# Performance work log

Measured on AMD Instinct MI355X. Metric: run time of the kernel, lower is better.

Reference implementation:

```python
import jax, jax.numpy as jnp
import numpy as np

IN, ENC, H = 60, 32, 64  # input feat, encoder out, LSTM hidden per direction


def _lstm_scan(x_tbf, W_ih, W_hh, b):
    """x_tbf: [T,B,ENC]. Returns final (h, c), each [B,H]. PyTorch gate order i,f,g,o."""
    B = x_tbf.shape[1]
    h0 = jnp.zeros((B, H), x_tbf.dtype)
    c0 = jnp.zeros((B, H), x_tbf.dtype)

    def step(carry, x_t):
        h, c = carry
        gates = x_t @ W_ih.T + h @ W_hh.T + b  # [B, 4H]
        i, f, g, o = jnp.split(gates, 4, axis=-1)
        c = jax.nn.sigmoid(f) * c + jax.nn.sigmoid(i) * jnp.tanh(g)
        h = jax.nn.sigmoid(o) * jnp.tanh(c)
        return (h, c), None

    (h_fin, c_fin), _ = jax.lax.scan(step, (h0, c0), x_tbf)
    return h_fin, c_fin


def setup_inputs() -> dict:
    key = jax.random.key(0)
    ks = jax.random.split(key, 10)
    B, T = 256, 4096
    s_enc = 1.0 / np.sqrt(IN)
    s_lstm = 1.0 / np.sqrt(H)
    s_fin = 1.0 / np.sqrt(2 * H)
    return {
        "c": jax.random.normal(ks[0], (B, T, IN), jnp.float32),
        "W_enc": jax.random.uniform(ks[1], (ENC, IN), jnp.float32, -s_enc, s_enc),
        "b_enc": jax.random.uniform(ks[2], (ENC,), jnp.float32, -s_enc, s_enc),
        "W_ih_f": jax.random.uniform(ks[3], (4 * H, ENC), jnp.float32, -s_lstm, s_lstm),
        "W_hh_f": jax.random.uniform(ks[4], (4 * H, H), jnp.float32, -s_lstm, s_lstm),
        "b_f": jax.random.uniform(ks[5], (4 * H,), jnp.float32, -s_lstm, s_lstm),
        "W_ih_b": jax.random.uniform(ks[6], (4 * H, ENC), jnp.float32, -s_lstm, s_lstm),
        "W_hh_b": jax.random.uniform(ks[7], (4 * H, H), jnp.float32, -s_lstm, s_lstm),
        "b_b": jax.random.uniform(ks[8], (4 * H,), jnp.float32, -s_lstm, s_lstm),
        "W_fin": jax.random.uniform(ks[9], (3, 2 * H), jnp.float32, -s_fin, s_fin),
        "b_fin": jnp.zeros((3,), jnp.float32),
    }


def reference(c, W_enc, b_enc, W_ih_f, W_hh_f, b_f, W_ih_b, W_hh_b, b_b, W_fin, b_fin):
    # SequenceWise linear encoder: [B,T,60] -> [B,T,32]
    x = c @ W_enc.T + b_enc
    x_tbf = jnp.transpose(x, (1, 0, 2))  # [T,B,ENC]
    # Bidirectional LSTM; original code unpacks (h_n, c_n) as (c, h),
    # so it feeds the final CELL states into final_fc — reproduce that.
    _, c_fwd = _lstm_scan(x_tbf, W_ih_f, W_hh_f, b_f)
    _, c_bwd = _lstm_scan(x_tbf[::-1], W_ih_b, W_hh_b, b_b)
    hidden = jnp.concatenate([c_fwd, c_bwd], axis=1)  # [B, 2H]
    return hidden @ W_fin.T + b_fin  # [B, 3]
```

## Files before the change

kernel.cpp:

```cpp
#include <hip/hip_runtime.h>
#include <hip/hip_bf16.h>

#define T_LEN 4096

typedef __attribute__((ext_vector_type(8))) short bfrag8;
typedef __attribute__((ext_vector_type(4))) float f32x4;

__device__ __forceinline__ void wg_barrier() {
  asm volatile("s_waitcnt lgkmcnt(0)\ns_barrier" ::: "memory");
}

__device__ __forceinline__ float fact(float x, float S, float A, float B) {
  float e = __builtin_amdgcn_exp2f(S * x);
  return A + B * __builtin_amdgcn_rcpf(1.0f + e);
}
__device__ __forceinline__ float ftanh(float x) {
  float e = __builtin_amdgcn_exp2f(2.8853900817779268f * x);
  return 1.0f - 2.0f * __builtin_amdgcn_rcpf(1.0f + e);
}
template <int SEL>
__device__ __forceinline__ float qb(float v) {
  union { float f; int i; } u;
  u.f = v;
  u.i = __builtin_amdgcn_mov_dpp(u.i, SEL * 0x55, 0xF, 0xF, true);
  return u.f;
}

__global__ void prep_enc(const float* __restrict__ W_enc,
                         __hip_bfloat16* __restrict__ Wencb) {
  int u = threadIdx.x;
  if (u < 32) {
    for (int k = 0; k < 64; ++k)
      Wencb[u * 64 + k] = __float2bfloat16(k < 60 ? W_enc[u * 60 + k] : 0.0f);
  }
}

__global__ __launch_bounds__(256) void encoder(const float* __restrict__ c,
                                               const __hip_bfloat16* __restrict__ Wencb,
                                               __hip_bfloat16* __restrict__ x) {
  const int lane = threadIdx.x & 63, wave = threadIdx.x >> 6;
  const int q = lane >> 4, l15 = lane & 15;
  const size_t r0 = ((size_t)blockIdx.x * 4 + wave) * 16;

  bfrag8 bf00 = *(const bfrag8*)(Wencb + (0 * 16 + l15) * 64 + 0 * 32 + q * 8);
  bfrag8 bf01 = *(const bfrag8*)(Wencb + (0 * 16 + l15) * 64 + 1 * 32 + q * 8);
  bfrag8 bf10 = *(const bfrag8*)(Wencb + (1 * 16 + l15) * 64 + 0 * 32 + q * 8);
  bfrag8 bf11 = *(const bfrag8*)(Wencb + (1 * 16 + l15) * 64 + 1 * 32 + q * 8);

  const float* cr = c + (r0 + l15) * 60;
  float4 a0 = *(const float4*)(cr + q * 8);
  float4 a1 = *(const float4*)(cr + q * 8 + 4);
  float4 a2 = *(const float4*)(cr + 32 + q * 8);
  float4 a3 = (q == 3) ? float4{0.f, 0.f, 0.f, 0.f}
                       : *(const float4*)(cr + 36 + q * 8);
  union { bfrag8 v; __hip_bfloat16 h[8]; } A0, A1;
  A0.h[0] = __float2bfloat16(a0.x); A0.h[1] = __float2bfloat16(a0.y);
  A0.h[2] = __float2bfloat16(a0.z); A0.h[3] = __float2bfloat16(a0.w);
  A0.h[4] = __float2bfloat16(a1.x); A0.h[5] = __float2bfloat16(a1.y);
  A0.h[6] = __float2bfloat16(a1.z); A0.h[7] = __float2bfloat16(a1.w);
  A1.h[0] = __float2bfloat16(a2.x); A1.h[1] = __float2bfloat16(a2.y);
  A1.h[2] = __float2bfloat16(a2.z); A1.h[3] = __float2bfloat16(a2.w);
  A1.h[4] = __float2bfloat16(a3.x); A1.h[5] = __float2bfloat16(a3.y);
  A1.h[6] = __float2bfloat16(a3.z); A1.h[7] = __float2bfloat16(a3.w);

  f32x4 acc0 = {0.f, 0.f, 0.f, 0.f}, acc1 = {0.f, 0.f, 0.f, 0.f};
  acc0 = __builtin_amdgcn_mfma_f32_16x16x32_bf16(A0.v, bf00, acc0, 0, 0, 0);
  acc1 = __builtin_amdgcn_mfma_f32_16x16x32_bf16(A0.v, bf10, acc1, 0, 0, 0);
  acc0 = __builtin_amdgcn_mfma_f32_16x16x32_bf16(A1.v, bf01, acc0, 0, 0, 0);
  acc1 = __builtin_amdgcn_mfma_f32_16x16x32_bf16(A1.v, bf11, acc1, 0, 0, 0);

#pragma unroll
  for (int r = 0; r < 4; ++r) {
    size_t row = r0 + q * 4 + r;
    x[row * 32 + l15]      = __float2bfloat16(acc0[r]);
    x[row * 32 + 16 + l15] = __float2bfloat16(acc1[r]);
  }
}

__global__ void prep_weights(const float* __restrict__ b_enc,
                             const float* __restrict__ W_ih_f,
                             const float* __restrict__ W_hh_f,
                             const float* __restrict__ b_f,
                             const float* __restrict__ W_ih_b,
                             const float* __restrict__ W_hh_b,
                             const float* __restrict__ b_b,
                             __hip_bfloat16* __restrict__ Wc,
                             float* __restrict__ biasc) {
  const int dir = blockIdx.x;
  const int np = threadIdx.x;
  const int tile = np >> 4, cc = np & 15;
  const int unit = tile * 4 + (cc >> 2);
  const int gate = cc & 3;
  const int no = gate * 64 + unit;
  const float* W_ih = dir ? W_ih_b : W_ih_f;
  const float* W_hh = dir ? W_hh_b : W_hh_f;
  const float* bv = dir ? b_b : b_f;
  __hip_bfloat16* row = Wc + (size_t)(dir * 256 + np) * 96;
#pragma unroll
  for (int k = 0; k < 32; ++k) row[k] = __float2bfloat16(W_ih[no * 32 + k]);
#pragma unroll
  for (int j = 0; j < 64; ++j) row[32 + j] = __float2bfloat16(W_hh[no * 64 + j]);
  float bb = bv[no];
#pragma unroll
  for (int e = 0; e < 32; ++e) bb += W_ih[no * 32 + e] * b_enc[e];
  biasc[dir * 256 + np] = bb;
}

__global__ __launch_bounds__(512, 2) void lstm_main(
    const __hip_bfloat16* __restrict__ x, const __hip_bfloat16* __restrict__ Wc,
    const float* __restrict__ biasc, float* __restrict__ cfin) {
  __shared__ __align__(16) short Hbuf[2][2][72];

  const int tid = threadIdx.x, lane = tid & 63, wave = tid >> 6;
  const int quad = lane >> 4, l15 = lane & 15;
  const int g = lane & 3;
  const int tsel = quad & 1;
  const int br = quad >> 1;
  const int unit = wave * 8 + tsel * 4 + (l15 >> 2);
  const int dir = (int)blockIdx.x & 1;
  const int pair = (int)blockIdx.x >> 1;
  const int b0 = pair * 2;
  const int bl = b0 + (l15 & 1);

  bfrag8 wf[2][3];
  float bias[2];
#pragma unroll
  for (int tl = 0; tl < 2; ++tl) {
    const int np = wave * 32 + tl * 16 + l15;
    const __hip_bfloat16* wr = Wc + (size_t)(dir * 256 + np) * 96 + quad * 8;
#pragma unroll
    for (int kt = 0; kt < 3; ++kt) wf[tl][kt] = *(const bfrag8*)(wr + kt * 32);
    bias[tl] = biasc[dir * 256 + np];
  }
  const f32x4 bv0 = {bias[0], bias[0], bias[0], bias[0]};
  const f32x4 bv1 = {bias[1], bias[1], bias[1], bias[1]};

  const bool isg = (g == 2);
  const float S = isg ? 2.8853900817779268f : -1.4426950408889634f;
  const float Aa = isg ? 1.0f : 0.0f;
  const float Bb = isg ? -2.0f : 1.0f;

  const __hip_bfloat16* xr = x + (size_t)bl * T_LEN * 32 + quad * 8;

  if (tid < 288) ((short*)Hbuf)[tid] = 0;

  bfrag8 xb[4];
#pragma unroll
  for (int qq = 0; qq < 4; ++qq) {
    int tp = dir ? (T_LEN - 1 - qq) : qq;
    xb[qq] = *(const bfrag8*)(xr + (size_t)tp * 32);
  }

  float cst = 0.f;
  wg_barrier();

#pragma unroll 4
  for (int t = 0; t < T_LEN; ++t) {
    const int cur = t & 1;
    const short* hb = &Hbuf[cur][l15 & 1][0];
    bfrag8 ahA = *(const bfrag8*)(hb + quad * 8);
    bfrag8 ahB = *(const bfrag8*)(hb + 32 + quad * 8);
    f32x4 a0 = __builtin_amdgcn_mfma_f32_16x16x32_bf16(xb[t & 3], wf[0][0], bv0, 0, 0, 0);
    f32x4 a1 = __builtin_amdgcn_mfma_f32_16x16x32_bf16(xb[t & 3], wf[1][0], bv1, 0, 0, 0);
    a0 = __builtin_amdgcn_mfma_f32_16x16x32_bf16(ahA, wf[0][1], a0, 0, 0, 0);
    a1 = __builtin_amdgcn_mfma_f32_16x16x32_bf16(ahA, wf[1][1], a1, 0, 0, 0);
    a0 = __builtin_amdgcn_mfma_f32_16x16x32_bf16(ahB, wf[0][2], a0, 0, 0, 0);
    a1 = __builtin_amdgcn_mfma_f32_16x16x32_bf16(ahB, wf[1][2], a1, 0, 0, 0);
    {
      int tn = t + 4; if (tn > T_LEN - 1) tn = T_LEN - 1;
      int tp = dir ? (T_LEN - 1 - tn) : tn;
      xb[t & 3] = *(const bfrag8*)(xr + (size_t)tp * 32);
    }
    float v0 = tsel ? a1[0] : a0[0];
    float v1 = tsel ? a1[1] : a0[1];
    float v = (quad & 2) ? v1 : v0;
    float act = fact(v, S, Aa, Bb);
    float gi = qb<0>(act), gf = qb<1>(act), gg = qb<2>(act), go = qb<3>(act);
    cst = gf * cst + gi * gg;
    float h = go * ftanh(cst);
    if (g == 0) *(__hip_bfloat16*)&Hbuf[cur ^ 1][br][unit] = __float2bfloat16(h);
    wg_barrier();
  }

  if (g == 0) cfin[(size_t)(dir * 256 + b0 + br) * 64 + unit] = cst;
}

__global__ void final_fc(const float* __restrict__ cfin,
                         const float* __restrict__ W_fin,
                         const float* __restrict__ b_fin,
                         float* __restrict__ out) {
  int b = threadIdx.x;
  const float* cf = cfin + (size_t)b * 64;
  const float* cb = cfin + (size_t)(256 + b) * 64;
  float a0 = b_fin[0], a1 = b_fin[1], a2 = b_fin[2];
  for (int u = 0; u < 64; ++u) {
    float vf = cf[u], vb = cb[u];
    a0 += W_fin[0 * 128 + u] * vf + W_fin[0 * 128 + 64 + u] * vb;
    a1 += W_fin[1 * 128 + u] * vf + W_fin[1 * 128 + 64 + u] * vb;
    a2 += W_fin[2 * 128 + u] * vf + W_fin[2 * 128 + 64 + u] * vb;
  }
  out[b * 3 + 0] = a0;
  out[b * 3 + 1] = a1;
  out[b * 3 + 2] = a2;
}

extern "C" void kernel_launch(void* const* d_in, const int* in_sizes, int n_in,
                              void* d_out, int out_size, void* d_ws, size_t ws_size,
                              hipStream_t stream) {
  (void)in_sizes; (void)n_in; (void)out_size; (void)ws_size;
  const float* c      = (const float*)d_in[0];
  const float* W_enc  = (const float*)d_in[1];
  const float* b_enc  = (const float*)d_in[2];
  const float* W_ih_f = (const float*)d_in[3];
  const float* W_hh_f = (const float*)d_in[4];
  const float* b_f    = (const float*)d_in[5];
  const float* W_ih_b = (const float*)d_in[6];
  const float* W_hh_b = (const float*)d_in[7];
  const float* b_b    = (const float*)d_in[8];
  const float* W_fin  = (const float*)d_in[9];
  const float* b_fin  = (const float*)d_in[10];
  float* out = (float*)d_out;

  char* ws = (char*)d_ws;
  __hip_bfloat16* x     = (__hip_bfloat16*)ws;
  __hip_bfloat16* Wc    = (__hip_bfloat16*)(ws + 67108864);
  float* biasc          = (float*)(ws + 67108864 + 98304);
  __hip_bfloat16* Wencb = (__hip_bfloat16*)(ws + 67108864 + 100352);
  float* cfin           = (float*)(ws + 67108864 + 104448);

  prep_enc<<<1, 32, 0, stream>>>(W_enc, Wencb);
  prep_weights<<<2, 256, 0, stream>>>(b_enc, W_ih_f, W_hh_f, b_f,
                                      W_ih_b, W_hh_b, b_b, Wc, biasc);
  encoder<<<16384, 256, 0, stream>>>(c, Wencb, x);
  lstm_main<<<256, 512, 0, stream>>>(x, Wc, biasc, cfin);
  final_fc<<<1, 256, 0, stream>>>(cfin, W_fin, b_fin, out);
}
```

Before: 1.324 ms.

## Fold encoder linear into LSTM input weights and read raw input directly

Precomputes W_ih·W_enc so the LSTM input projection consumes the raw 60-feature input directly, removing the separate encoder kernel and its intermediate bf16 activation buffer. The recurrent kernel now loads fp32 rows of c, converts them to bf16 in-loop, and does one extra pair of MFMAs per step (K=64 instead of 32). This trades a full encoder pass and its global write/read for more per-step loads, conversions and MFMA work on the serial critical path, and a slightly different rounding order.

Result: slower. 4.794 ms (+262.2%).

```diff
diff --git a/kernel.cpp b/kernel.cpp
--- a/kernel.cpp
+++ b/kernel.cpp
@@ -26,58 +26,17 @@
   return u.f;
 }
 
-__global__ void prep_enc(const float* __restrict__ W_enc,
-                         __hip_bfloat16* __restrict__ Wencb) {
-  int u = threadIdx.x;
-  if (u < 32) {
-    for (int k = 0; k < 64; ++k)
-      Wencb[u * 64 + k] = __float2bfloat16(k < 60 ? W_enc[u * 60 + k] : 0.0f);
-  }
-}
-
-__global__ __launch_bounds__(256) void encoder(const float* __restrict__ c,
-                                               const __hip_bfloat16* __restrict__ Wencb,
-                                               __hip_bfloat16* __restrict__ x) {
-  const int lane = threadIdx.x & 63, wave = threadIdx.x >> 6;
-  const int q = lane >> 4, l15 = lane & 15;
-  const size_t r0 = ((size_t)blockIdx.x * 4 + wave) * 16;
-
-  bfrag8 bf00 = *(const bfrag8*)(Wencb + (0 * 16 + l15) * 64 + 0 * 32 + q * 8);
-  bfrag8 bf01 = *(const bfrag8*)(Wencb + (0 * 16 + l15) * 64 + 1 * 32 + q * 8);
-  bfrag8 bf10 = *(const bfrag8*)(Wencb + (1 * 16 + l15) * 64 + 0 * 32 + q * 8);
-  bfrag8 bf11 = *(const bfrag8*)(Wencb + (1 * 16 + l15) * 64 + 1 * 32 + q * 8);
-
-  const float* cr = c + (r0 + l15) * 60;
-  float4 a0 = *(const float4*)(cr + q * 8);
-  float4 a1 = *(const float4*)(cr + q * 8 + 4);
-  float4 a2 = *(const float4*)(cr + 32 + q * 8);
-  float4 a3 = (q == 3) ? float4{0.f, 0.f, 0.f, 0.f}
-                       : *(const float4*)(cr + 36 + q * 8);
-  union { bfrag8 v; __hip_bfloat16 h[8]; } A0, A1;
-  A0.h[0] = __float2bfloat16(a0.x); A0.h[1] = __float2bfloat16(a0.y);
-  A0.h[2] = __float2bfloat16(a0.z); A0.h[3] = __float2bfloat16(a0.w);
-  A0.h[4] = __float2bfloat16(a1.x); A0.h[5] = __float2bfloat16(a1.y);
-  A0.h[6] = __float2bfloat16(a1.z); A0.h[7] = __float2bfloat16(a1.w);
-  A1.h[0] = __float2bfloat16(a2.x); A1.h[1] = __float2bfloat16(a2.y);
-  A1.h[2] = __float2bfloat16(a2.z); A1.h[3] = __float2bfloat16(a2.w);
-  A1.h[4] = __float2bfloat16(a3.x); A1.h[5] = __float2bfloat16(a3.y);
-  A1.h[6] = __float2bfloat16(a3.z); A1.h[7] = __float2bfloat16(a3.w);
-
-  f32x4 acc0 = {0.f, 0.f, 0.f, 0.f}, acc1 = {0.f, 0.f, 0.f, 0.f};
-  acc0 = __builtin_amdgcn_mfma_f32_16x16x32_bf16(A0.v, bf00, acc0, 0, 0, 0);
-  acc1 = __builtin_amdgcn_mfma_f32_16x16x32_bf16(A0.v, bf10, acc1, 0, 0, 0);
-  acc0 = __builtin_amdgcn_mfma_f32_16x16x32_bf16(A1.v, bf01, acc0, 0, 0, 0);
-  acc1 = __builtin_amdgcn_mfma_f32_16x16x32_bf16(A1.v, bf11, acc1, 0, 0, 0);
-
-#pragma unroll
-  for (int r = 0; r < 4; ++r) {
-    size_t row = r0 + q * 4 + r;
-    x[row * 32 + l15]      = __float2bfloat16(acc0[r]);
-    x[row * 32 + 16 + l15] = __float2bfloat16(acc1[r]);
-  }
-}
-
-__global__ void prep_weights(const float* __restrict__ b_enc,
+__device__ __forceinline__ void loadc(float4 (&r)[4], const float* row, int q) {
+  const float* pr = row + q * 8;
+  r[0] = *(const float4*)(pr);
+  r[1] = *(const float4*)(pr + 4);
+  r[2] = *(const float4*)(row + 32 + q * 8);
+  r[3] = float4{0.f, 0.f, 0.f, 0.f};
+  if (q < 3) r[3] = *(const float4*)(row + 36 + q * 8);
+}
+
+__global__ void prep_weights(const float* __restrict__ W_enc,
+                             const float* __restrict__ b_enc,
                              const float* __restrict__ W_ih_f,
                              const float* __restrict__ W_hh_f,
                              const float* __restrict__ b_f,
@@ -95,11 +54,16 @@
   const float* W_ih = dir ? W_ih_b : W_ih_f;
   const float* W_hh = dir ? W_hh_b : W_hh_f;
   const float* bv = dir ? b_b : b_f;
-  __hip_bfloat16* row = Wc + (size_t)(dir * 256 + np) * 96;
-#pragma unroll
-  for (int k = 0; k < 32; ++k) row[k] = __float2bfloat16(W_ih[no * 32 + k]);
-#pragma unroll
-  for (int j = 0; j < 64; ++j) row[32 + j] = __float2bfloat16(W_hh[no * 64 + j]);
+  __hip_bfloat16* row = Wc + (size_t)(dir * 256 + np) * 128;
+  for (int k = 0; k < 60; ++k) {
+    float s = 0.f;
+#pragma unroll
+    for (int e = 0; e < 32; ++e) s += W_ih[no * 32 + e] * W_enc[e * 60 + k];
+    row[k] = __float2bfloat16(s);
+  }
+  row[60] = row[61] = row[62] = row[63] = __float2bfloat16(0.f);
+#pragma unroll
+  for (int j = 0; j < 64; ++j) row[64 + j] = __float2bfloat16(W_hh[no * 64 + j]);
   float bb = bv[no];
 #pragma unroll
   for (int e = 0; e < 32; ++e) bb += W_ih[no * 32 + e] * b_enc[e];
@@ -107,7 +71,7 @@
 }
 
 __global__ __launch_bounds__(512, 2) void lstm_main(
-    const __hip_bfloat16* __restrict__ x, const __hip_bfloat16* __restrict__ Wc,
+    const float* __restrict__ c, const __hip_bfloat16* __restrict__ Wc,
     const float* __restrict__ biasc, float* __restrict__ cfin) {
   __shared__ __align__(16) short Hbuf[2][2][72];
 
@@ -122,14 +86,16 @@
   const int b0 = pair * 2;
   const int bl = b0 + (l15 & 1);
 
-  bfrag8 wf[2][3];
+  bfrag8 wx[2][2], wh[2][2];
   float bias[2];
 #pragma unroll
   for (int tl = 0; tl < 2; ++tl) {
     const int np = wave * 32 + tl * 16 + l15;
-    const __hip_bfloat16* wr = Wc + (size_t)(dir * 256 + np) * 96 + quad * 8;
-#pragma unroll
-    for (int kt = 0; kt < 3; ++kt) wf[tl][kt] = *(const bfrag8*)(wr + kt * 32);
+    const __hip_bfloat16* wr = Wc + (size_t)(dir * 256 + np) * 128 + quad * 8;
+    wx[tl][0] = *(const bfrag8*)(wr);
+    wx[tl][1] = *(const bfrag8*)(wr + 32);
+    wh[tl][0] = *(const bfrag8*)(wr + 64);
+    wh[tl][1] = *(const bfrag8*)(wr + 96);
     bias[tl] = biasc[dir * 256 + np];
   }
   const f32x4 bv0 = {bias[0], bias[0], bias[0], bias[0]};
@@ -140,16 +106,17 @@
   const float Aa = isg ? 1.0f : 0.0f;
   const float Bb = isg ? -2.0f : 1.0f;
 
-  const __hip_bfloat16* xr = x + (size_t)bl * T_LEN * 32 + quad * 8;
+  const float* p = c + ((size_t)bl * T_LEN + (dir ? (T_LEN - 1) : 0)) * 60;
+  const int sstep = dir ? -60 : 60;
+
+  float4 r[4][4];
+#pragma unroll
+  for (int qq = 0; qq < 4; ++qq) {
+    loadc(r[qq], p, quad);
+    p += sstep;
+  }
 
   if (tid < 288) ((short*)Hbuf)[tid] = 0;
-
-  bfrag8 xb[4];
-#pragma unroll
-  for (int qq = 0; qq < 4; ++qq) {
-    int tp = dir ? (T_LEN - 1 - qq) : qq;
-    xb[qq] = *(const bfrag8*)(xr + (size_t)tp * 32);
-  }
 
   float cst = 0.f;
   wg_barrier();
@@ -160,16 +127,30 @@
     const short* hb = &Hbuf[cur][l15 & 1][0];
     bfrag8 ahA = *(const bfrag8*)(hb + quad * 8);
     bfrag8 ahB = *(const bfrag8*)(hb + 32 + quad * 8);
-    f32x4 a0 = __builtin_amdgcn_mfma_f32_16x16x32_bf16(xb[t & 3], wf[0][0], bv0, 0, 0, 0);
-    f32x4 a1 = __builtin_amdgcn_mfma_f32_16x16x32_bf16(xb[t & 3], wf[1][0], bv1, 0, 0, 0);
-    a0 = __builtin_amdgcn_mfma_f32_16x16x32_bf16(ahA, wf[0][1], a0, 0, 0, 0);
-    a1 = __builtin_amdgcn_mfma_f32_16x16x32_bf16(ahA, wf[1][1], a1, 0, 0, 0);
-    a0 = __builtin_amdgcn_mfma_f32_16x16x32_bf16(ahB, wf[0][2], a0, 0, 0, 0);
-    a1 = __builtin_amdgcn_mfma_f32_16x16x32_bf16(ahB, wf[1][2], a1, 0, 0, 0);
+    union { bfrag8 v; __hip_bfloat16 h[8]; } X0, X1;
     {
-      int tn = t + 4; if (tn > T_LEN - 1) tn = T_LEN - 1;
-      int tp = dir ? (T_LEN - 1 - tn) : tn;
-      xb[t & 3] = *(const bfrag8*)(xr + (size_t)tp * 32);
+      float4 q0 = r[t & 3][0], q1 = r[t & 3][1];
+      float4 q2 = r[t & 3][2], q3 = r[t & 3][3];
+      X0.h[0] = __float2bfloat16(q0.x); X0.h[1] = __float2bfloat16(q0.y);
+      X0.h[2] = __float2bfloat16(q0.z); X0.h[3] = __float2bfloat16(q0.w);
+      X0.h[4] = __float2bfloat16(q1.x); X0.h[5] = __float2bfloat16(q1.y);
+      X0.h[6] = __float2bfloat16(q1.z); X0.h[7] = __float2bfloat16(q1.w);
+      X1.h[0] = __float2bfloat16(q2.x); X1.h[1] = __float2bfloat16(q2.y);
+      X1.h[2] = __float2bfloat16(q2.z); X1.h[3] = __float2bfloat16(q2.w);
+      X1.h[4] = __float2bfloat16(q3.x); X1.h[5] = __float2bfloat16(q3.y);
+      X1.h[6] = __float2bfloat16(q3.z); X1.h[7] = __float2bfloat16(q3.w);
+    }
+    f32x4 a0 = __builtin_amdgcn_mfma_f32_16x16x32_bf16(X0.v, wx[0][0], bv0, 0, 0, 0);
+    f32x4 a1 = __builtin_amdgcn_mfma_f32_16x16x32_bf16(X0.v, wx[1][0], bv1, 0, 0, 0);
+    a0 = __builtin_amdgcn_mfma_f32_16x16x32_bf16(X1.v, wx[0][1], a0, 0, 0, 0);
+    a1 = __builtin_amdgcn_mfma_f32_16x16x32_bf16(X1.v, wx[1][1], a1, 0, 0, 0);
+    a0 = __builtin_amdgcn_mfma_f32_16x16x32_bf16(ahA, wh[0][0], a0, 0, 0, 0);
+    a1 = __builtin_amdgcn_mfma_f32_16x16x32_bf16(ahA, wh[1][0], a1, 0, 0, 0);
+    a0 = __builtin_amdgcn_mfma_f32_16x16x32_bf16(ahB, wh[0][1], a0, 0, 0, 0);
+    a1 = __builtin_amdgcn_mfma_f32_16x16x32_bf16(ahB, wh[1][1], a1, 0, 0, 0);
+    if (t < T_LEN - 4) {
+      loadc(r[t & 3], p, quad);
+      p += sstep;
     }
     float v0 = tsel ? a1[0] : a0[0];
     float v1 = tsel ? a1[1] : a0[1];
@@ -222,16 +203,12 @@
   float* out = (float*)d_out;
 
   char* ws = (char*)d_ws;
-  __hip_bfloat16* x     = (__hip_bfloat16*)ws;
-  __hip_bfloat16* Wc    = (__hip_bfloat16*)(ws + 67108864);
-  float* biasc          = (float*)(ws + 67108864 + 98304);
-  __hip_bfloat16* Wencb = (__hip_bfloat16*)(ws + 67108864 + 100352);
-  float* cfin           = (float*)(ws + 67108864 + 104448);
-
-  prep_enc<<<1, 32, 0, stream>>>(W_enc, Wencb);
-  prep_weights<<<2, 256, 0, stream>>>(b_enc, W_ih_f, W_hh_f, b_f,
+  __hip_bfloat16* Wc = (__hip_bfloat16*)ws;
+  float* biasc       = (float*)(ws + 131072);
+  float* cfin        = (float*)(ws + 131072 + 2048);
+
+  prep_weights<<<2, 256, 0, stream>>>(W_enc, b_enc, W_ih_f, W_hh_f, b_f,
                                       W_ih_b, W_hh_b, b_b, Wc, biasc);
-  encoder<<<16384, 256, 0, stream>>>(c, Wencb, x);
-  lstm_main<<<256, 512, 0, stream>>>(x, Wc, biasc, cfin);
+  lstm_main<<<256, 512, 0, stream>>>(c, Wc, biasc, cfin);
   final_fc<<<1, 256, 0, stream>>>(cfin, W_fin, b_fin, out);
 }
```

## Precompute next-step input projection off critical path and fold encoder weight prep into kernel

Applied to the files above, without the earlier changes.

The LSTM loop now computes the input-projection MFMAs for step t+1 after writing h and before the barrier, so each recurrent step's critical path holds only the two hidden-state MFMA pairs. Separately, the prep_enc kernel is removed. Each encoder block now converts W_enc to bf16 in shared memory, which drops one launch but repeats the conversion in every block and adds a __syncthreads.

Result: no change. 1.312 ms (-0.9%).

```diff
diff --git a/kernel.cpp b/kernel.cpp
--- a/kernel.cpp
+++ b/kernel.cpp
@@ -26,26 +26,24 @@
   return u.f;
 }
 
-__global__ void prep_enc(const float* __restrict__ W_enc,
-                         __hip_bfloat16* __restrict__ Wencb) {
-  int u = threadIdx.x;
-  if (u < 32) {
-    for (int k = 0; k < 64; ++k)
-      Wencb[u * 64 + k] = __float2bfloat16(k < 60 ? W_enc[u * 60 + k] : 0.0f);
-  }
-}
-
 __global__ __launch_bounds__(256) void encoder(const float* __restrict__ c,
-                                               const __hip_bfloat16* __restrict__ Wencb,
+                                               const float* __restrict__ W_enc,
                                                __hip_bfloat16* __restrict__ x) {
+  __shared__ __align__(16) __hip_bfloat16 Wl[32 * 64];
+  {
+    const int i0 = threadIdx.x * 8;
+    const int u = i0 >> 6, k0 = i0 & 63;
+#pragma unroll
+    for (int j = 0; j < 8; ++j) {
+      int kk = k0 + j;
+      Wl[i0 + j] = __float2bfloat16(kk < 60 ? W_enc[u * 60 + kk] : 0.0f);
+    }
+  }
+  __syncthreads();
+
   const int lane = threadIdx.x & 63, wave = threadIdx.x >> 6;
   const int q = lane >> 4, l15 = lane & 15;
   const size_t r0 = ((size_t)blockIdx.x * 4 + wave) * 16;
-
-  bfrag8 bf00 = *(const bfrag8*)(Wencb + (0 * 16 + l15) * 64 + 0 * 32 + q * 8);
-  bfrag8 bf01 = *(const bfrag8*)(Wencb + (0 * 16 + l15) * 64 + 1 * 32 + q * 8);
-  bfrag8 bf10 = *(const bfrag8*)(Wencb + (1 * 16 + l15) * 64 + 0 * 32 + q * 8);
-  bfrag8 bf11 = *(const bfrag8*)(Wencb + (1 * 16 + l15) * 64 + 1 * 32 + q * 8);
 
   const float* cr = c + (r0 + l15) * 60;
   float4 a0 = *(const float4*)(cr + q * 8);
@@ -53,6 +51,12 @@
   float4 a2 = *(const float4*)(cr + 32 + q * 8);
   float4 a3 = (q == 3) ? float4{0.f, 0.f, 0.f, 0.f}
                        : *(const float4*)(cr + 36 + q * 8);
+
+  bfrag8 bf00 = *(const bfrag8*)(Wl + (0 * 16 + l15) * 64 + 0 * 32 + q * 8);
+  bfrag8 bf01 = *(const bfrag8*)(Wl + (0 * 16 + l15) * 64 + 1 * 32 + q * 8);
+  bfrag8 bf10 = *(const bfrag8*)(Wl + (1 * 16 + l15) * 64 + 0 * 32 + q * 8);
+  bfrag8 bf11 = *(const bfrag8*)(Wl + (1 * 16 + l15) * 64 + 1 * 32 + q * 8);
+
   union { bfrag8 v; __hip_bfloat16 h[8]; } A0, A1;
   A0.h[0] = __float2bfloat16(a0.x); A0.h[1] = __float2bfloat16(a0.y);
   A0.h[2] = __float2bfloat16(a0.z); A0.h[3] = __float2bfloat16(a0.w);
@@ -151,6 +155,9 @@
     xb[qq] = *(const bfrag8*)(xr + (size_t)tp * 32);
   }
 
+  f32x4 ax0 = __builtin_amdgcn_mfma_f32_16x16x32_bf16(xb[0], wf[0][0], bv0, 0, 0, 0);
+  f32x4 ax1 = __builtin_amdgcn_mfma_f32_16x16x32_bf16(xb[0], wf[1][0], bv1, 0, 0, 0);
+
   float cst = 0.f;
   wg_barrier();
 
@@ -160,10 +167,8 @@
     const short* hb = &Hbuf[cur][l15 & 1][0];
     bfrag8 ahA = *(const bfrag8*)(hb + quad * 8);
     bfrag8 ahB = *(const bfrag8*)(hb + 32 + quad * 8);
-    f32x4 a0 = __builtin_amdgcn_mfma_f32_16x16x32_bf16(xb[t & 3], wf[0][0], bv0, 0, 0, 0);
-    f32x4 a1 = __builtin_amdgcn_mfma_f32_16x16x32_bf16(xb[t & 3], wf[1][0], bv1, 0, 0, 0);
-    a0 = __builtin_amdgcn_mfma_f32_16x16x32_bf16(ahA, wf[0][1], a0, 0, 0, 0);
-    a1 = __builtin_amdgcn_mfma_f32_16x16x32_bf16(ahA, wf[1][1], a1, 0, 0, 0);
+    f32x4 a0 = __builtin_amdgcn_mfma_f32_16x16x32_bf16(ahA, wf[0][1], ax0, 0, 0, 0);
+    f32x4 a1 = __builtin_amdgcn_mfma_f32_16x16x32_bf16(ahA, wf[1][1], ax1, 0, 0, 0);
     a0 = __builtin_amdgcn_mfma_f32_16x16x32_bf16(ahB, wf[0][2], a0, 0, 0, 0);
     a1 = __builtin_amdgcn_mfma_f32_16x16x32_bf16(ahB, wf[1][2], a1, 0, 0, 0);
     {
@@ -179,6 +184,8 @@
     cst = gf * cst + gi * gg;
     float h = go * ftanh(cst);
     if (g == 0) *(__hip_bfloat16*)&Hbuf[cur ^ 1][br][unit] = __float2bfloat16(h);
+    ax0 = __builtin_amdgcn_mfma_f32_16x16x32_bf16(xb[(t + 1) & 3], wf[0][0], bv0, 0, 0, 0);
+    ax1 = __builtin_amdgcn_mfma_f32_16x16x32_bf16(xb[(t + 1) & 3], wf[1][0], bv1, 0, 0, 0);
     wg_barrier();
   }
 
@@ -222,16 +229,14 @@
   float* out = (float*)d_out;
 
   char* ws = (char*)d_ws;
-  __hip_bfloat16* x     = (__hip_bfloat16*)ws;
-  __hip_bfloat16* Wc    = (__hip_bfloat16*)(ws + 67108864);
-  float* biasc          = (float*)(ws + 67108864 + 98304);
-  __hip_bfloat16* Wencb = (__hip_bfloat16*)(ws + 67108864 + 100352);
-  float* cfin           = (float*)(ws + 67108864 + 104448);
-
-  prep_enc<<<1, 32, 0, stream>>>(W_enc, Wencb);
+  __hip_bfloat16* x  = (__hip_bfloat16*)ws;
+  __hip_bfloat16* Wc = (__hip_bfloat16*)(ws + 67108864);
+  float* biasc       = (float*)(ws + 67108864 + 98304);
+  float* cfin        = (float*)(ws + 67108864 + 100352);
+
   prep_weights<<<2, 256, 0, stream>>>(b_enc, W_ih_f, W_hh_f, b_f,
                                       W_ih_b, W_hh_b, b_b, Wc, biasc);
-  encoder<<<16384, 256, 0, stream>>>(c, Wencb, x);
+  encoder<<<16384, 256, 0, stream>>>(c, W_enc, x);
   lstm_main<<<256, 512, 0, stream>>>(x, Wc, biasc, cfin);
   final_fc<<<1, 256, 0, stream>>>(cfin, W_fin, b_fin, out);
 }
```
